# Kernel tuning notes

Hardware: AMD Instinct MI355X
Metric: run time of the kernel (lower is better)

The kernel has to match this reference:

```python
import jax, jax.numpy as jnp
from jax import lax
import numpy as np

NUM_LABELS = 64
ENC_DIM = 256
C = 128            # channels
C2 = 2 * C         # trunk width
OUT_DIM = 512
LAYERS = [(3, 1), (3, 2), (3, 4), (3, 8), (3, 16)]
RF = 1 + sum((k - 1) * d for k, d in LAYERS)   # 63
MAX_T = 48
PAD, START, STOP = 0, 5, 6
BATCH, T_ENC = 8, 64


def setup_inputs() -> dict:
    key = jax.random.key(0)
    ks = jax.random.split(key, 20)

    def w(k, shape, fan_in):
        return (jax.random.normal(k, shape, jnp.float32) * np.sqrt(2.0 / fan_in)).astype(jnp.float32)

    def b(k, shape):
        return 1e-4 * jax.random.normal(k, shape, jnp.float32)

    L = len(LAYERS)
    return {
        'encoded_seq': jax.random.normal(ks[0], (BATCH, ENC_DIM, T_ENC), jnp.float32),
        'embed':  w(ks[1], (NUM_LABELS, C2), NUM_LABELS),
        'w_in':   w(ks[2], (C2, C2), C2),      'b_in':  b(ks[3], (C2,)),
        'w_enc':  w(ks[4], (ENC_DIM, C2), ENC_DIM), 'b_enc': b(ks[5], (C2,)),
        'res_w1': w(ks[6], (L, C2, C), C2),    'res_b1': b(ks[7], (L, C)),
        'res_wd': w(ks[8], (L, 3, C, C), 3 * C), 'res_bd': b(ks[9], (L, C)),
        'res_w2': w(ks[10], (L, C, C2), C),    'res_b2': b(ks[11], (L, C2)),
        'w_o1':   w(ks[12], (C2, OUT_DIM), C2), 'b_o1': b(ks[13], (OUT_DIM,)),
        'w_o2':   w(ks[14], (OUT_DIM, NUM_LABELS), OUT_DIM), 'b_o2': b(ks[15], (NUM_LABELS,)),
    }


def _decode(encoded_seq, embed, w_in, b_in, w_enc, b_enc,
            res_w1, res_b1, res_wd, res_bd, res_w2, res_b2,
            w_o1, b_o1, w_o2, b_o2):
    B = encoded_seq.shape[0]
    # left-pad encoding with rf-1 zeros (torch code leaves these uninitialized; zeros used here)
    encoded_pad = jnp.concatenate(
        [jnp.zeros((B, ENC_DIM, RF - 1), encoded_seq.dtype), encoded_seq], axis=2)

    def linear(labels, enc_win):
        # labels: (B, RF) int32; enc_win: (B, ENC_DIM, RF)
        x = embed[labels]                                     # (B, RF, C2)
        x = x @ w_in + b_in                                   # input 1x1 conv
        x = x + jnp.einsum('bct,cd->btd', enc_win, w_enc) + b_enc
        for i, (kk, d) in enumerate(LAYERS):                  # ReLU residual blocks
            h = jax.nn.relu(x)
            h = jax.nn.relu(h @ res_w1[i] + res_b1[i])        # 2c -> c
            h = lax.conv_general_dilated(                     # causal dilated conv c -> c
                h, res_wd[i], window_strides=(1,), padding=[((kk - 1) * d, 0)],
                rhs_dilation=(d,), dimension_numbers=('NWC', 'WIO', 'NWC')) + res_bd[i]
            h = jax.nn.relu(h)
            x = x + (h @ res_w2[i] + res_b2[i])               # c -> 2c, residual
        o = jax.nn.relu(x @ w_o1 + b_o1) @ w_o2 + b_o2        # (B, RF, NUM_LABELS)
        return o[:, -1, :]                                    # last timestep only

    def step(labels, k):
        enc_win = lax.dynamic_slice(encoded_pad, (0, 0, k), (B, ENC_DIM, RF))
        logit = linear(labels, enc_win)                       # (B, NUM_LABELS)
        nxt = jnp.argmax(logit, axis=-1).astype(jnp.int32)
        labels = jnp.concatenate([labels[:, 1:], nxt[:, None]], axis=1)
        return labels, (logit, nxt)

    init_labels = jnp.concatenate(
        [jnp.full((B, RF - 1), PAD, jnp.int32), jnp.full((B, 1), START, jnp.int32)], axis=1)
    _, (logits, nexts) = lax.scan(step, init_labels, jnp.arange(MAX_T))
    logits = jnp.transpose(logits, (1, 2, 0))                 # (B, NUM_LABELS, T)
    stopped = jnp.cumsum((nexts == STOP).astype(jnp.int32), axis=0) >= 1  # (T, B), incl. current step
    lengths = (MAX_T - stopped.sum(axis=0)).astype(jnp.int32)
    return logits, lengths


def reference(encoded_seq, embed, w_in, b_in, w_enc, b_enc,
              res_w1, res_b1, res_wd, res_bd, res_w2, res_b2,
              w_o1, b_o1, w_o2, b_o2):
    return _decode(encoded_seq, embed, w_in, b_in, w_enc, b_enc,
                   res_w1, res_b1, res_wd, res_bd, res_w2, res_b2,
                   w_o1, b_o1, w_o2, b_o2)
```

## Files before the change

### kernel.cpp

```cpp
#include <hip/hip_runtime.h>
#include <hip/hip_bf16.h>

#define NUM_LABELS 64
#define ENC_DIM 256
#define CC 128
#define C2 256
#define OUT_DIM 512
#define NLAYERS 5
#define RF 63
#define MAX_T 48
#define BATCH 8
#define T_ENC 64
#define LAB_PAD 0
#define LAB_START 5
#define LAB_STOP 6

__global__ __launch_bounds__(256) void pre_kernel(
    const float* __restrict__ enc,
    const float* __restrict__ embed,
    const float* __restrict__ w_in,
    const float* __restrict__ b_in,
    const float* __restrict__ w_enc,
    const float* __restrict__ b_enc,
    float* __restrict__ E2,
    float* __restrict__ encp)
{
    const int t = threadIdx.x;
    const int blk = blockIdx.x;
    if (blk < NUM_LABELS) {
        float acc = b_in[t];
        const float* e = embed + blk * C2;
        for (int j = 0; j < C2; ++j) acc += e[j] * w_in[j * C2 + t];
        E2[blk * C2 + t] = acc;
    } else {
        const int idx = blk - NUM_LABELS;
        const int b = idx / MAX_T;
        const int k = idx % MAX_T;
        float acc = b_enc[t];
        const float* ecol = enc + b * ENC_DIM * T_ENC + k;
        for (int c = 0; c < ENC_DIM; ++c) acc += ecol[c * T_ENC] * w_enc[c * C2 + t];
        encp[idx * C2 + t] = acc;
    }
}

__global__ __launch_bounds__(256) void prefix_kernel(
    const float* __restrict__ embed, const float* __restrict__ w_in,
    const float* __restrict__ b_in,  const float* __restrict__ b_enc,
    const float* __restrict__ w1,    const float* __restrict__ b1,
    const float* __restrict__ wd,    const float* __restrict__ bd,
    const float* __restrict__ w2,    const float* __restrict__ b2,
    float* __restrict__ h0out)
{
    const int t = threadIdx.x;
    __shared__ float x[C2];
    __shared__ float r[C2];
    __shared__ float h[CC];
    __shared__ float hr[CC];

    {
        float acc = b_in[t] + b_enc[t];
        const float* e = embed + LAB_PAD * C2;
        for (int j = 0; j < C2; ++j) acc += e[j] * w_in[j * C2 + t];
        x[t] = acc;
    }
    __syncthreads();

    for (int i = 0; i < NLAYERS; ++i) {
        r[t] = fmaxf(x[t], 0.f);
        __syncthreads();
        if (t < CC) {
            float a = b1[i * CC + t];
            const float* W = w1 + (i * C2) * CC + t;
            for (int j = 0; j < C2; ++j) a += r[j] * W[j * CC];
            float hv = fmaxf(a, 0.f);
            h[t] = hv;
            h0out[i * CC + t] = hv;
        }
        __syncthreads();
        if (t < CC) {
            float a = bd[i * CC + t];
            const float* W0 = wd + ((i * 3 + 0) * CC) * CC + t;
            const float* W1 = wd + ((i * 3 + 1) * CC) * CC + t;
            const float* W2 = wd + ((i * 3 + 2) * CC) * CC + t;
            for (int c = 0; c < CC; ++c) {
                float wsum = W0[c * CC] + W1[c * CC] + W2[c * CC];
                a += h[c] * wsum;
            }
            hr[t] = fmaxf(a, 0.f);
        }
        __syncthreads();
        {
            float a = b2[i * C2 + t];
            const float* W = w2 + (i * CC) * C2 + t;
            for (int c = 0; c < CC; ++c) a += hr[c] * W[c * C2];
            x[t] += a;
        }
        __syncthreads();
    }
}

__global__ __launch_bounds__(256) void decode_kernel(
    const float* __restrict__ w1,
    const float* __restrict__ b1,
    const float* __restrict__ wd,
    const float* __restrict__ bd,
    const float* __restrict__ w2,
    const float* __restrict__ b2,
    const float* __restrict__ wo1,
    const float* __restrict__ bo1,
    const float* __restrict__ wo2,
    const float* __restrict__ bo2,
    const float* __restrict__ E2,
    const float* __restrict__ encp,
    const float* __restrict__ h0g,
    float* __restrict__ out)
{
    const int b = blockIdx.x;
    const int t = threadIdx.x;

    __shared__ float ring0[3 * CC];
    __shared__ float ring1[5 * CC];
    __shared__ float ring2[9 * CC];
    __shared__ float ring3[17 * CC];
    __shared__ float ring4[33 * CC];
    __shared__ float h0s[NLAYERS * CC];
    __shared__ float x[C2];
    __shared__ float r[C2];
    __shared__ float h[CC];
    __shared__ float hr[CC];
    __shared__ float part[256];
    __shared__ float u[OUT_DIM];
    __shared__ float lg[NUM_LABELS];
    __shared__ int s_lab;
    __shared__ int s_stop;

    float* rings[NLAYERS] = { ring0, ring1, ring2, ring3, ring4 };
    const int rsz[NLAYERS] = { 3, 5, 9, 17, 33 };

    for (int idx = t; idx < NLAYERS * CC; idx += 256) h0s[idx] = h0g[idx];
    if (t == 0) { s_lab = LAB_START; s_stop = MAX_T; }
    __syncthreads();

    for (int k = 0; k < MAX_T; ++k) {
        const int lab = s_lab;
        x[t] = E2[lab * C2 + t] + encp[(b * MAX_T + k) * C2 + t];
        r[t] = fmaxf(x[t], 0.f);
        __syncthreads();

        for (int i = 0; i < NLAYERS; ++i) {
            const int d = 1 << i;
            {
                const int c = t & (CC - 1);
                const int half = t >> 7;
                float a = 0.f;
                const float* W = w1 + (i * C2 + half * CC) * CC + c;
                const float* rr = r + half * CC;
                for (int j = 0; j < CC; ++j) a += rr[j] * W[j * CC];
                part[t] = a;
            }
            __syncthreads();
            if (t < CC) {
                float hv = fmaxf(part[t] + part[t + CC] + b1[i * CC + t], 0.f);
                h[t] = hv;
                rings[i][(k % rsz[i]) * CC + t] = hv;
            }
            __syncthreads();
            {
                const int c = t & (CC - 1);
                const int half = t >> 7;
                const float* tap1 = (k >= d)     ? &rings[i][((k - d)     % rsz[i]) * CC] : &h0s[i * CC];
                const float* tap0 = (k >= 2 * d) ? &rings[i][((k - 2 * d) % rsz[i]) * CC] : &h0s[i * CC];
                const float* W0 = wd + ((i * 3 + 0) * CC) * CC + c;
                const float* W1 = wd + ((i * 3 + 1) * CC) * CC + c;
                const float* W2 = wd + ((i * 3 + 2) * CC) * CC + c;
                float a = 0.f;
                const int c0 = half * 64, c1 = c0 + 64;
                for (int cc = c0; cc < c1; ++cc) {
                    a += h[cc]    * W2[cc * CC];
                    a += tap1[cc] * W1[cc * CC];
                    a += tap0[cc] * W0[cc * CC];
                }
                part[t] = a;
            }
            __syncthreads();
            if (t < CC) {
                hr[t] = fmaxf(part[t] + part[t + CC] + bd[i * CC + t], 0.f);
            }
            __syncthreads();
            {
                float a = b2[i * C2 + t];
                const float* W = w2 + (i * CC) * C2 + t;
                for (int c = 0; c < CC; ++c) a += hr[c] * W[c * C2];
                float xv = x[t] + a;
                x[t] = xv;
                r[t] = fmaxf(xv, 0.f);
            }
            __syncthreads();
        }

        for (int rep = 0; rep < 2; ++rep) {
            const int o = t + rep * 256;
            float a = bo1[o];
            const float* W = wo1 + o;
            for (int j = 0; j < C2; ++j) a += x[j] * W[j * OUT_DIM];
            u[o] = fmaxf(a, 0.f);
        }
        __syncthreads();
        {
            const int l = t & (NUM_LABELS - 1);
            const int q = t >> 6;
            float a = 0.f;
            const float* W = wo2 + l;
            const int o0 = q * 128, o1 = o0 + 128;
            for (int o = o0; o < o1; ++o) a += u[o] * W[o * NUM_LABELS];
            part[t] = a;
        }
        __syncthreads();
        if (t < NUM_LABELS) {
            float a = part[t] + part[t + 64] + part[t + 128] + part[t + 192] + bo2[t];
            lg[t] = a;
            out[(b * NUM_LABELS + t) * MAX_T + k] = a;
        }
        __syncthreads();
        if (t == 0) {
            float best = lg[0];
            int bi = 0;
            for (int l = 1; l < NUM_LABELS; ++l) {
                if (lg[l] > best) { best = lg[l]; bi = l; }
            }
            s_lab = bi;
            if (bi == LAB_STOP && s_stop == MAX_T) s_stop = k;
        }
        __syncthreads();
    }

    if (t == 0) {
        out[BATCH * NUM_LABELS * MAX_T + b] = (float)s_stop;
    }
}

extern "C" void kernel_launch(void* const* d_in, const int* in_sizes, int n_in,
                              void* d_out, int out_size, void* d_ws, size_t ws_size,
                              hipStream_t stream) {
    const float* enc   = (const float*)d_in[0];
    const float* embed = (const float*)d_in[1];
    const float* w_in  = (const float*)d_in[2];
    const float* b_in  = (const float*)d_in[3];
    const float* w_enc = (const float*)d_in[4];
    const float* b_enc = (const float*)d_in[5];
    const float* w1    = (const float*)d_in[6];
    const float* b1    = (const float*)d_in[7];
    const float* wd    = (const float*)d_in[8];
    const float* bd    = (const float*)d_in[9];
    const float* w2    = (const float*)d_in[10];
    const float* b2    = (const float*)d_in[11];
    const float* wo1   = (const float*)d_in[12];
    const float* bo1   = (const float*)d_in[13];
    const float* wo2   = (const float*)d_in[14];
    const float* bo2   = (const float*)d_in[15];
    float* out = (float*)d_out;
    float* ws  = (float*)d_ws;

    float* E2   = ws;
    float* encp = ws + 16384;
    float* h0   = ws + 16384 + 98304;

    pre_kernel<<<NUM_LABELS + BATCH * MAX_T, 256, 0, stream>>>(
        enc, embed, w_in, b_in, w_enc, b_enc, E2, encp);
    prefix_kernel<<<1, 256, 0, stream>>>(
        embed, w_in, b_in, b_enc, w1, b1, wd, bd, w2, b2, h0);
    decode_kernel<<<BATCH, 256, 0, stream>>>(
        w1, b1, wd, bd, w2, b2, wo1, bo1, wo2, bo2, E2, encp, h0, out);
}
```

Measured before the change: 2.751 ms.

## Repack weights into float4 row-interleaved layout and double decode threads to 512

Adds a repack kernel that interleaves every four input rows of each weight matrix into float4, so the decode kernel loads weights with 16-byte vector loads and reads activations as float4 from LDS. The decode block grows from 256 to 512 threads, splitting each reduction four ways with partial sums in shared memory. The serial argmax over 64 labels becomes a wavefront shuffle reduction. Five extra launches per call rebuild the repacked weights in the workspace.

```diff
diff --git a/kernel.cpp b/kernel.cpp
--- a/kernel.cpp
+++ b/kernel.cpp
@@ -7,7 +7,6 @@
 #define C2 256
 #define OUT_DIM 512
 #define NLAYERS 5
-#define RF 63
 #define MAX_T 48
 #define BATCH 8
 #define T_ENC 64
@@ -16,14 +15,10 @@
 #define LAB_STOP 6
 
 __global__ __launch_bounds__(256) void pre_kernel(
-    const float* __restrict__ enc,
-    const float* __restrict__ embed,
-    const float* __restrict__ w_in,
-    const float* __restrict__ b_in,
-    const float* __restrict__ w_enc,
-    const float* __restrict__ b_enc,
-    float* __restrict__ E2,
-    float* __restrict__ encp)
+    const float* __restrict__ enc, const float* __restrict__ embed,
+    const float* __restrict__ w_in, const float* __restrict__ b_in,
+    const float* __restrict__ w_enc, const float* __restrict__ b_enc,
+    float* __restrict__ E2, float* __restrict__ encp)
 {
     const int t = threadIdx.x;
     const int blk = blockIdx.x;
@@ -82,10 +77,8 @@
             const float* W0 = wd + ((i * 3 + 0) * CC) * CC + t;
             const float* W1 = wd + ((i * 3 + 1) * CC) * CC + t;
             const float* W2 = wd + ((i * 3 + 2) * CC) * CC + t;
-            for (int c = 0; c < CC; ++c) {
-                float wsum = W0[c * CC] + W1[c * CC] + W2[c * CC];
-                a += h[c] * wsum;
-            }
+            for (int c = 0; c < CC; ++c)
+                a += h[c] * (W0[c * CC] + W1[c * CC] + W2[c * CC]);
             hr[t] = fmaxf(a, 0.f);
         }
         __syncthreads();
@@ -99,144 +92,186 @@
     }
 }
 
-__global__ __launch_bounds__(256) void decode_kernel(
-    const float* __restrict__ w1,
-    const float* __restrict__ b1,
-    const float* __restrict__ wd,
-    const float* __restrict__ bd,
-    const float* __restrict__ w2,
-    const float* __restrict__ b2,
-    const float* __restrict__ wo1,
-    const float* __restrict__ bo1,
-    const float* __restrict__ wo2,
-    const float* __restrict__ bo2,
-    const float* __restrict__ E2,
-    const float* __restrict__ encp,
-    const float* __restrict__ h0g,
-    float* __restrict__ out)
+__global__ __launch_bounds__(256) void repack4_kernel(
+    const float* __restrict__ src, float4* __restrict__ dst, int OUT)
+{
+    const int p = blockIdx.x * 256 + threadIdx.x;
+    const int c = p % OUT;
+    const int jb = p / OUT;
+    const float* s = src + (size_t)jb * 4 * OUT + c;
+    float4 v;
+    v.x = s[0 * OUT]; v.y = s[1 * OUT]; v.z = s[2 * OUT]; v.w = s[3 * OUT];
+    dst[p] = v;
+}
+
+__global__ __launch_bounds__(512) void decode_kernel(
+    const float4* __restrict__ w1c,  const float* __restrict__ b1,
+    const float4* __restrict__ wdc,  const float* __restrict__ bd,
+    const float4* __restrict__ w2c,  const float* __restrict__ b2,
+    const float4* __restrict__ wo1c, const float* __restrict__ bo1,
+    const float4* __restrict__ wo2c, const float* __restrict__ bo2,
+    const float* __restrict__ E2, const float* __restrict__ encp,
+    const float* __restrict__ h0g, float* __restrict__ out)
 {
     const int b = blockIdx.x;
     const int t = threadIdx.x;
 
-    __shared__ float ring0[3 * CC];
-    __shared__ float ring1[5 * CC];
-    __shared__ float ring2[9 * CC];
-    __shared__ float ring3[17 * CC];
-    __shared__ float ring4[33 * CC];
-    __shared__ float h0s[NLAYERS * CC];
-    __shared__ float x[C2];
-    __shared__ float r[C2];
-    __shared__ float h[CC];
-    __shared__ float hr[CC];
-    __shared__ float part[256];
-    __shared__ float u[OUT_DIM];
-    __shared__ float lg[NUM_LABELS];
-    __shared__ int s_lab;
-    __shared__ int s_stop;
+    __shared__ alignas(16) float ring0[3 * CC];
+    __shared__ alignas(16) float ring1[5 * CC];
+    __shared__ alignas(16) float ring2[9 * CC];
+    __shared__ alignas(16) float ring3[17 * CC];
+    __shared__ alignas(16) float ring4[33 * CC];
+    __shared__ alignas(16) float h0s[NLAYERS * CC];
+    __shared__ alignas(16) float xs[C2];
+    __shared__ alignas(16) float rs[C2];
+    __shared__ alignas(16) float hr[CC];
+    __shared__ alignas(16) float us[OUT_DIM];
+    __shared__ float part[512];
+    __shared__ int s_lab, s_stop;
 
     float* rings[NLAYERS] = { ring0, ring1, ring2, ring3, ring4 };
-    const int rsz[NLAYERS] = { 3, 5, 9, 17, 33 };
-
-    for (int idx = t; idx < NLAYERS * CC; idx += 256) h0s[idx] = h0g[idx];
+    const int rszc[NLAYERS] = { 3, 5, 9, 17, 33 };
+
+    for (int idx = t; idx < NLAYERS * CC; idx += 512) h0s[idx] = h0g[idx];
     if (t == 0) { s_lab = LAB_START; s_stop = MAX_T; }
     __syncthreads();
 
     for (int k = 0; k < MAX_T; ++k) {
-        const int lab = s_lab;
-        x[t] = E2[lab * C2 + t] + encp[(b * MAX_T + k) * C2 + t];
-        r[t] = fmaxf(x[t], 0.f);
-        __syncthreads();
-
+        if (t < C2) {
+            float xv = E2[s_lab * C2 + t] + encp[(b * MAX_T + k) * C2 + t];
+            xs[t] = xv;
+            rs[t] = fmaxf(xv, 0.f);
+        }
+        __syncthreads();
+
+#pragma unroll
         for (int i = 0; i < NLAYERS; ++i) {
             const int d = 1 << i;
+            const int rsz = rszc[i];
+            const int cslot = k % rsz;
+            float* rng = rings[i];
+
             {
-                const int c = t & (CC - 1);
-                const int half = t >> 7;
-                float a = 0.f;
-                const float* W = w1 + (i * C2 + half * CC) * CC + c;
-                const float* rr = r + half * CC;
-                for (int j = 0; j < CC; ++j) a += rr[j] * W[j * CC];
-                part[t] = a;
+                const int c = t & 127, g = t >> 7;
+                const float4* W = w1c + (i * 64 + g * 16) * 128 + c;
+                const float* rp = rs + g * 64;
+                float acc = 0.f;
+#pragma unroll
+                for (int m = 0; m < 16; ++m) {
+                    float4 w = W[m * 128];
+                    float4 v = *(const float4*)(rp + m * 4);
+                    acc += w.x * v.x + w.y * v.y + w.z * v.z + w.w * v.w;
+                }
+                part[t] = acc;
             }
             __syncthreads();
             if (t < CC) {
-                float hv = fmaxf(part[t] + part[t + CC] + b1[i * CC + t], 0.f);
-                h[t] = hv;
-                rings[i][(k % rsz[i]) * CC + t] = hv;
-            }
-            __syncthreads();
+                float hv = fmaxf(part[t] + part[t + 128] + part[t + 256] + part[t + 384]
+                                 + b1[i * CC + t], 0.f);
+                rng[cslot * CC + t] = hv;
+            }
+            __syncthreads();
+
             {
-                const int c = t & (CC - 1);
-                const int half = t >> 7;
-                const float* tap1 = (k >= d)     ? &rings[i][((k - d)     % rsz[i]) * CC] : &h0s[i * CC];
-                const float* tap0 = (k >= 2 * d) ? &rings[i][((k - 2 * d) % rsz[i]) * CC] : &h0s[i * CC];
-                const float* W0 = wd + ((i * 3 + 0) * CC) * CC + c;
-                const float* W1 = wd + ((i * 3 + 1) * CC) * CC + c;
-                const float* W2 = wd + ((i * 3 + 2) * CC) * CC + c;
-                float a = 0.f;
-                const int c0 = half * 64, c1 = c0 + 64;
-                for (int cc = c0; cc < c1; ++cc) {
-                    a += h[cc]    * W2[cc * CC];
-                    a += tap1[cc] * W1[cc * CC];
-                    a += tap0[cc] * W0[cc * CC];
+                const int c = t & 127, g = t >> 7;
+                const float* cur = rng + cslot * CC;
+                const float* tp1 = (k >= d)     ? rng + ((k - d) % rsz) * CC     : h0s + i * CC;
+                const float* tp0 = (k >= 2 * d) ? rng + ((k - 2 * d) % rsz) * CC : h0s + i * CC;
+                const float4* W0 = wdc + ((i * 3 + 0) * 32 + g * 8) * 128 + c;
+                const float4* W1 = wdc + ((i * 3 + 1) * 32 + g * 8) * 128 + c;
+                const float4* W2 = wdc + ((i * 3 + 2) * 32 + g * 8) * 128 + c;
+                float acc = 0.f;
+#pragma unroll
+                for (int m = 0; m < 8; ++m) {
+                    float4 wa = W0[m * 128];
+                    float4 wb = W1[m * 128];
+                    float4 wc = W2[m * 128];
+                    float4 a0 = *(const float4*)(tp0 + g * 32 + m * 4);
+                    float4 a1 = *(const float4*)(tp1 + g * 32 + m * 4);
+                    float4 a2 = *(const float4*)(cur + g * 32 + m * 4);
+                    acc += wa.x * a0.x + wa.y * a0.y + wa.z * a0.z + wa.w * a0.w;
+                    acc += wb.x * a1.x + wb.y * a1.y + wb.z * a1.z + wb.w * a1.w;
+                    acc += wc.x * a2.x + wc.y * a2.y + wc.z * a2.z + wc.w * a2.w;
                 }
-                part[t] = a;
+                part[t] = acc;
             }
             __syncthreads();
             if (t < CC) {
-                hr[t] = fmaxf(part[t] + part[t + CC] + bd[i * CC + t], 0.f);
-            }
-            __syncthreads();
+                hr[t] = fmaxf(part[t] + part[t + 128] + part[t + 256] + part[t + 384]
+                              + bd[i * CC + t], 0.f);
+            }
+            __syncthreads();
+
             {
-                float a = b2[i * C2 + t];
-                const float* W = w2 + (i * CC) * C2 + t;
-                for (int c = 0; c < CC; ++c) a += hr[c] * W[c * C2];
-                float xv = x[t] + a;
-                x[t] = xv;
-                r[t] = fmaxf(xv, 0.f);
-            }
-            __syncthreads();
-        }
-
-        for (int rep = 0; rep < 2; ++rep) {
-            const int o = t + rep * 256;
-            float a = bo1[o];
-            const float* W = wo1 + o;
-            for (int j = 0; j < C2; ++j) a += x[j] * W[j * OUT_DIM];
-            u[o] = fmaxf(a, 0.f);
-        }
-        __syncthreads();
+                const int c = t & 255, g = t >> 8;
+                const float4* W = w2c + (i * 32 + g * 16) * 256 + c;
+                const float* hp = hr + g * 64;
+                float acc = 0.f;
+#pragma unroll
+                for (int m = 0; m < 16; ++m) {
+                    float4 w = W[m * 256];
+                    float4 v = *(const float4*)(hp + m * 4);
+                    acc += w.x * v.x + w.y * v.y + w.z * v.z + w.w * v.w;
+                }
+                part[t] = acc;
+            }
+            __syncthreads();
+            if (t < C2) {
+                float xv = xs[t] + part[t] + part[t + 256] + b2[i * C2 + t];
+                xs[t] = xv;
+                rs[t] = fmaxf(xv, 0.f);
+            }
+            __syncthreads();
+        }
+
         {
-            const int l = t & (NUM_LABELS - 1);
-            const int q = t >> 6;
-            float a = 0.f;
-            const float* W = wo2 + l;
-            const int o0 = q * 128, o1 = o0 + 128;
-            for (int o = o0; o < o1; ++o) a += u[o] * W[o * NUM_LABELS];
-            part[t] = a;
+            float acc = bo1[t];
+            const float4* W = wo1c + t;
+#pragma unroll 16
+            for (int jb = 0; jb < 64; ++jb) {
+                float4 w = W[jb * 512];
+                float4 v = *(const float4*)(xs + jb * 4);
+                acc += w.x * v.x + w.y * v.y + w.z * v.z + w.w * v.w;
+            }
+            us[t] = fmaxf(acc, 0.f);
+        }
+        __syncthreads();
+
+        {
+            const int c = t & 63, g = t >> 6;
+            const float4* W = wo2c + (g * 16) * 64 + c;
+            const float* up = us + g * 64;
+            float acc = 0.f;
+#pragma unroll
+            for (int m = 0; m < 16; ++m) {
+                float4 w = W[m * 64];
+                float4 v = *(const float4*)(up + m * 4);
+                acc += w.x * v.x + w.y * v.y + w.z * v.z + w.w * v.w;
+            }
+            part[t] = acc;
         }
         __syncthreads();
         if (t < NUM_LABELS) {
-            float a = part[t] + part[t + 64] + part[t + 128] + part[t + 192] + bo2[t];
-            lg[t] = a;
-            out[(b * NUM_LABELS + t) * MAX_T + k] = a;
-        }
-        __syncthreads();
-        if (t == 0) {
-            float best = lg[0];
-            int bi = 0;
-            for (int l = 1; l < NUM_LABELS; ++l) {
-                if (lg[l] > best) { best = lg[l]; bi = l; }
-            }
-            s_lab = bi;
-            if (bi == LAB_STOP && s_stop == MAX_T) s_stop = k;
+            float v = part[t] + part[t + 64] + part[t + 128] + part[t + 192]
+                    + part[t + 256] + part[t + 320] + part[t + 384] + part[t + 448]
+                    + bo2[t];
+            out[(b * NUM_LABELS + t) * MAX_T + k] = v;
+            float bv = v; int bi = t;
+#pragma unroll
+            for (int off = 32; off; off >>= 1) {
+                float ov = __shfl_xor(bv, off);
+                int oi = __shfl_xor(bi, off);
+                if (ov > bv || (ov == bv && oi < bi)) { bv = ov; bi = oi; }
+            }
+            if (t == 0) {
+                s_lab = bi;
+                if (bi == LAB_STOP && s_stop == MAX_T) s_stop = k;
+            }
         }
         __syncthreads();
     }
 
-    if (t == 0) {
-        out[BATCH * NUM_LABELS * MAX_T + b] = (float)s_stop;
-    }
+    if (t == 0) out[BATCH * NUM_LABELS * MAX_T + b] = (float)s_stop;
 }
 
 extern "C" void kernel_launch(void* const* d_in, const int* in_sizes, int n_in,
@@ -259,16 +294,26 @@
     const float* wo2   = (const float*)d_in[14];
     const float* bo2   = (const float*)d_in[15];
     float* out = (float*)d_out;
-    float* ws  = (float*)d_ws;
-
-    float* E2   = ws;
-    float* encp = ws + 16384;
-    float* h0   = ws + 16384 + 98304;
+    float* wsf = (float*)d_ws;
+
+    float* E2   = wsf;
+    float* encp = wsf + 16384;
+    float* h0   = wsf + 16384 + 98304;
+    float4* w1c  = (float4*)(wsf + 115328);
+    float4* wdc  = w1c + 40960;
+    float4* w2c  = wdc + 61440;
+    float4* wo1c = w2c + 40960;
+    float4* wo2c = wo1c + 32768;
 
     pre_kernel<<<NUM_LABELS + BATCH * MAX_T, 256, 0, stream>>>(
         enc, embed, w_in, b_in, w_enc, b_enc, E2, encp);
     prefix_kernel<<<1, 256, 0, stream>>>(
         embed, w_in, b_in, b_enc, w1, b1, wd, bd, w2, b2, h0);
-    decode_kernel<<<BATCH, 256, 0, stream>>>(
-        w1, b1, wd, bd, w2, b2, wo1, bo1, wo2, bo2, E2, encp, h0, out);
-}
+    repack4_kernel<<<160, 256, 0, stream>>>(w1, w1c, 128);
+    repack4_kernel<<<240, 256, 0, stream>>>(wd, wdc, 128);
+    repack4_kernel<<<160, 256, 0, stream>>>(w2, w2c, 256);
+    repack4_kernel<<<128, 256, 0, stream>>>(wo1, wo1c, 512);
+    repack4_kernel<<<32, 256, 0, stream>>>(wo2, wo2c, 64);
+    decode_kernel<<<BATCH, 512, 0, stream>>>(
+        w1c, b1, wdc, bd, w2c, b2, wo1c, bo1, wo2c, bo2, E2, encp, h0, out);
+}
```

Result: slower. 3.687 ms (+34.0%).
